# Optimization experiments

Hardware: AMD Instinct MI355X
Metric: run time of the kernel (lower is better)

## Reference

```python
import jax, jax.numpy as jnp
import numpy as np

N = 4096        # nodes
E = 65536       # edges (avg degree 16)
L = 64          # latent_dims
K = 256         # kernel_dims
ED = 6          # edge_dims
DEPTH = 2


def _gelu(x):
    # torch.nn.GELU / F.gelu default = exact erf form
    return jax.nn.gelu(x, approximate=False)


def setup_inputs() -> dict:
    key = jax.random.key(0)
    ks = jax.random.split(key, 12)
    u = lambda k, shape, fan: jax.random.uniform(k, shape, jnp.float32, -1.0, 1.0) / np.sqrt(fan)
    return {
        "nodes": jax.random.normal(ks[0], (N, L), jnp.float32),
        "edge_index": jax.random.randint(ks[1], (2, E), 0, N, jnp.int32),
        "edge_attr": jax.random.uniform(ks[2], (E, ED), jnp.float32),
        # DenseNet kernel MLP: ED -> K -> K -> L*L (GELU between layers)
        "W1": u(ks[3], (ED, K), ED), "b1": jnp.zeros((K,), jnp.float32),
        "W2": u(ks[4], (K, K), K),  "b2": jnp.zeros((K,), jnp.float32),
        "W3": u(ks[5], (K, L * L), K), "b3": jnp.zeros((L * L,), jnp.float32),
        # NNConv root linear (no bias) + conv bias
        "W_root": u(ks[6], (L, L), L),
        "bias": jnp.zeros((L,), jnp.float32),
    }


def reference(nodes, edge_index, edge_attr, W1, b1, W2, b2, W3, b3, W_root, bias):
    src, dst = edge_index[0], edge_index[1]
    # Edge-conditioned dynamic weights (depend only on edge_attr -> compute once)
    h = _gelu(edge_attr @ W1 + b1)          # [E, K]
    h = _gelu(h @ W2 + b2)                  # [E, K]
    W_edge = (h @ W3 + b3).reshape(E, L, L) # [E, L_in, L_out]

    def conv(x):
        msg = jnp.einsum('ei,eio->eo', x[src], W_edge)          # gather + per-edge matmul
        agg = jax.ops.segment_sum(msg, dst, num_segments=N)     # scatter-add to dst
        return agg + x @ W_root + bias

    x = nodes
    for idx in range(DEPTH):
        x = conv(x)
        if idx < DEPTH - 1:
            x = _gelu(x)
    return x
```

## Files before the change

kernel.cpp:

```cpp
#include <hip/hip_runtime.h>
#include <math.h>

#define NN 4096
#define NE 65536
#define LL 64
#define KK 256
#define ED 6
#define MAXSUPER 6144

typedef __bf16 bf16_t;
typedef __attribute__((ext_vector_type(4))) __bf16 bf16x4;
typedef __attribute__((ext_vector_type(8))) __bf16 bf16x8;
typedef __attribute__((ext_vector_type(4))) float f32x4;
typedef __attribute__((ext_vector_type(16))) float f32x16;

#define OFF_CNT    ((size_t)0)
#define OFF_DESC   ((size_t)16384)
#define OFF_AGG0   ((size_t)147456)
#define OFF_AGG1   ((size_t)1196032)
#define ZERO_BYTES ((size_t)2244608)
#define OFF_CURSOR ((size_t)2244608)
#define OFF_SORTED ((size_t)2260992)
#define OFF_W2R    ((size_t)2785280)
#define OFF_W3RR   ((size_t)2916352)
#define OFF_Q0     ((size_t)5013504)
#define OFF_Q1     ((size_t)6062080)
#define OFF_X1F    ((size_t)7110656)
#define OFF_X0BF   ((size_t)8159232)
#define OFF_X1BF   ((size_t)8683520)
#define OFF_H      ((size_t)9207808)
#define OFF_P      ((size_t)42762240)

__device__ __forceinline__ float gelu_f(float x) {
    return 0.5f * x * (1.0f + erff(x * 0.7071067811865476f));
}
__device__ __forceinline__ bf16_t f2bf(float x) { return (bf16_t)x; }

__global__ void k_hist(const int* __restrict__ ei, int* __restrict__ cnt) {
    int e = blockIdx.x * 256 + threadIdx.x;
    atomicAdd(&cnt[ei[e]], 1);
}

__global__ void k_scan(const int* __restrict__ cnt, int* __restrict__ cursor,
                       int4* __restrict__ descs) {
    __shared__ int pd[1024], pc[1024];
    int t = threadIdx.x;
    int deg[4]; int sd = 0, sc = 0;
#pragma unroll
    for (int j = 0; j < 4; j++) {
        deg[j] = cnt[t * 4 + j];
        sd += deg[j];
        sc += (deg[j] + 31) >> 5;
    }
    pd[t] = sd; pc[t] = sc;
    __syncthreads();
    for (int off = 1; off < 1024; off <<= 1) {
        int vd = 0, vc = 0;
        if (t >= off) { vd = pd[t - off]; vc = pc[t - off]; }
        __syncthreads();
        pd[t] += vd; pc[t] += vc;
        __syncthreads();
    }
    int rd = (t > 0) ? pd[t - 1] : 0;
    int rc = (t > 0) ? pc[t - 1] : 0;
    for (int j = 0; j < 4; j++) {
        int v = t * 4 + j, d = deg[j];
        cursor[v] = rd;
        int nch = (d + 31) >> 5;
        for (int c = 0; c < nch; c++) {
            int rem = d - c * 32;
            descs[rc + c] = make_int4(v, rd + c * 32, rem < 32 ? rem : 32, 0);
        }
        rc += nch; rd += d;
    }
}

__global__ void __launch_bounds__(256) k_fuse3(
        const int* __restrict__ ei, int* __restrict__ cursor, int2* __restrict__ sorted,
        const float* __restrict__ W3, bf16_t* __restrict__ W3rr,
        const float* __restrict__ W2, bf16_t* __restrict__ W2r,
        const float* __restrict__ attr, const float* __restrict__ W1,
        const float* __restrict__ b1, bf16_t* __restrict__ a1,
        const float* __restrict__ x, const float* __restrict__ b3,
        bf16_t* __restrict__ xbf, float* __restrict__ Q) {
    __shared__ float smem[4096];
    int bid = blockIdx.x, tid = threadIdx.x;
    if (bid < 256) {
        int e = bid * 256 + tid;
        int s = ei[e], d = ei[NE + e];
        int pos = atomicAdd(&cursor[s], 1);
        sorted[pos] = make_int2(e, d);
    } else if (bid < 512) {
        int k0 = bid - 256;
        for (int idx = tid; idx < 4096; idx += 256)
            smem[idx] = W3[(size_t)k0 * 4096 + idx];
        __syncthreads();
        int sbase = (2 * (k0 >> 4)) * 512 + (((k0 >> 3) & 1) * 32) * 8 + (k0 & 7);
#pragma unroll
        for (int m = 0; m < 2; m++) {
            int w = m * 256 + tid;
            int o = w >> 3, ib = w & 7;
            int s = sbase + (o >> 5) * 512 + (o & 31) * 8;
            int f = (s >> 4) * 1024 + (ib >> 2) * 512 + (ib & 3) * 128 + (s & 15) * 8;
            bf16x8 pk;
#pragma unroll
            for (int j = 0; j < 8; j++) pk[j] = f2bf(smem[(ib * 8 + j) * 64 + o]);
            *(bf16x8*)(W3rr + f) = pk;
        }
    } else if (bid < 768) {
        int t = (bid - 512) * 256 + tid;
        int kk = t >> 13, nn = (t >> 9) & 15, lane = (t >> 3) & 63, j = t & 7;
        int k = kk * 32 + (lane >> 4) * 8 + j;
        int n = nn * 16 + (lane & 15);
        W2r[t] = f2bf(W2[k * 256 + n]);
    } else if (bid < 1792) {
        float* sa = smem;
        int e0 = (bid - 768) * 64;
        for (int i = tid; i < 64 * ED; i += 256) sa[i] = attr[(size_t)e0 * ED + i];
        int col4 = (tid & 63) * 4;
        float w[ED][4], bb[4];
#pragma unroll
        for (int j = 0; j < ED; j++)
#pragma unroll
            for (int c = 0; c < 4; c++) w[j][c] = W1[j * 256 + col4 + c];
#pragma unroll
        for (int c = 0; c < 4; c++) bb[c] = b1[col4 + c];
        __syncthreads();
        int esub = tid >> 6;
#pragma unroll 1
        for (int eg = 0; eg < 16; eg++) {
            int el = eg * 4 + esub;
            float av[ED];
#pragma unroll
            for (int j = 0; j < ED; j++) av[j] = sa[el * ED + j];
            bf16x4 ov;
#pragma unroll
            for (int c = 0; c < 4; c++) {
                float acc = bb[c];
#pragma unroll
                for (int j = 0; j < ED; j++) acc += av[j] * w[j][c];
                ov[c] = f2bf(gelu_f(acc));
            }
            *(bf16x4*)(a1 + (size_t)(e0 + el) * 256 + col4) = ov;
        }
    } else {
        int v = (bid - 1792) * 4 + (tid >> 6);
        int o = tid & 63;
        float xv = x[v * 64 + o];
        smem[tid] = xv;
        xbf[v * 64 + o] = f2bf(xv);
        __syncthreads();
        const float* sx = smem + (tid >> 6) * 64;
        float q = 0.0f;
#pragma unroll 8
        for (int i = 0; i < 64; i++) q += sx[i] * b3[i * 64 + o];
        Q[v * 64 + o] = q;
    }
}

__device__ __forceinline__ void pgemm_body(const bf16_t* __restrict__ xbf,
                                           const bf16_t* __restrict__ W3rr,
                                           bf16_t* __restrict__ P,
                                           bf16_t* __restrict__ sw_wave,
                                           int strip, int rg) {
    int wave = threadIdx.x >> 6, lane = threadIdx.x & 63;
    int col = lane & 15, quad = lane >> 4;
    int half = lane >> 5, l5 = lane & 31;
    bf16_t* sw = sw_wave + wave * 4224;
    bf16x8 b[16][2];
#pragma unroll
    for (int nn = 0; nn < 16; nn++) {
        int sn = strip * 16 + nn;
#pragma unroll
        for (int ki = 0; ki < 2; ki++)
            b[nn][ki] = *(const bf16x8*)(W3rr + (size_t)(sn * 2 + ki) * 512 + lane * 8);
    }
#pragma unroll 1
    for (int rt = 0; rt < 4; rt++) {
        int rowbase = rg * 256 + wave * 64 + rt * 16;
        const bf16_t* arow = xbf + (size_t)(rowbase + col) * 64;
        bf16x8 a0 = *(const bf16x8*)(arow + quad * 8);
        bf16x8 a1v = *(const bf16x8*)(arow + 32 + quad * 8);
#pragma unroll
        for (int nn = 0; nn < 16; nn++) {
            f32x4 acc;
#pragma unroll
            for (int r = 0; r < 4; r++) acc[r] = 0.0f;
            acc = __builtin_amdgcn_mfma_f32_16x16x32_bf16(b[nn][0], a0, acc, 0, 0, 0);
            acc = __builtin_amdgcn_mfma_f32_16x16x32_bf16(b[nn][1], a1v, acc, 0, 0, 0);
            bf16x4 pk;
#pragma unroll
            for (int r = 0; r < 4; r++) pk[r] = f2bf(acc[r]);
            *(bf16x4*)(sw + col * 264 + nn * 16 + quad * 4) = pk;
        }
        __builtin_amdgcn_wave_barrier();
#pragma unroll
        for (int i = 0; i < 8; i++) {
            int r2 = 2 * i + half;
            bf16x8 vb = *(const bf16x8*)(sw + r2 * 264 + l5 * 8);
            *(bf16x8*)(P + (size_t)(rowbase + r2) * 16384 + strip * 256 + l5 * 8) = vb;
        }
        __builtin_amdgcn_wave_barrier();
    }
}

__global__ void __launch_bounds__(256, 2) k_fuse4(const bf16_t* __restrict__ xbf,
                                                  const bf16_t* __restrict__ W3rr,
                                                  bf16_t* __restrict__ P,
                                                  const bf16_t* __restrict__ a1,
                                                  const bf16_t* __restrict__ W2r,
                                                  const float* __restrict__ b2,
                                                  bf16_t* __restrict__ h) {
    __shared__ bf16_t sB[16896];
    if (blockIdx.x < 1024) {
        pgemm_body(xbf, W3rr, P, sB, blockIdx.x & 63, blockIdx.x >> 6);
    } else {
        int tid = threadIdx.x;
        int wave = tid >> 6, lane = tid & 63, col = lane & 15, quad = lane >> 4;
        int base = (blockIdx.x - 1024) * 128 + wave * 32;
        bf16x8 a[2][8];
#pragma unroll
        for (int t = 0; t < 2; t++) {
            const bf16_t* arow = a1 + (size_t)(base + t * 16 + col) * 256;
#pragma unroll
            for (int kk = 0; kk < 8; kk++)
                a[t][kk] = *(const bf16x8*)(arow + kk * 32 + quad * 8);
        }
#pragma unroll 1
        for (int p = 0; p < 4; p++) {
#pragma unroll
            for (int it = 0; it < 8; it++) {
                int c = it * 256 + tid;
                int fl = c >> 6;
                int e = (c & 63) * 8;
                int kk = fl >> 2, nnl = fl & 3;
                *(bf16x8*)(sB + fl * 512 + e) =
                    *(const bf16x8*)(W2r + (size_t)(kk * 16 + p * 4 + nnl) * 512 + e);
            }
            __syncthreads();
#pragma unroll
            for (int nnl = 0; nnl < 4; nnl++) {
                f32x4 acc0, acc1;
#pragma unroll
                for (int r = 0; r < 4; r++) { acc0[r] = 0.0f; acc1[r] = 0.0f; }
#pragma unroll
                for (int kk = 0; kk < 8; kk++) {
                    bf16x8 b = *(const bf16x8*)(sB + (kk * 4 + nnl) * 512 + lane * 8);
                    acc0 = __builtin_amdgcn_mfma_f32_16x16x32_bf16(a[0][kk], b, acc0, 0, 0, 0);
                    acc1 = __builtin_amdgcn_mfma_f32_16x16x32_bf16(a[1][kk], b, acc1, 0, 0, 0);
                }
                int ncol = (p * 4 + nnl) * 16 + col;
                float bv = b2[ncol];
#pragma unroll
                for (int r = 0; r < 4; r++) {
                    int row0 = base + quad * 4 + r;
                    h[(size_t)row0 * 256 + ncol] = f2bf(gelu_f(acc0[r] + bv));
                    h[(size_t)(row0 + 16) * 256 + ncol] = f2bf(gelu_f(acc1[r] + bv));
                }
            }
            __syncthreads();
        }
    }
}

__global__ void __launch_bounds__(256, 2) k_pgemm(const bf16_t* __restrict__ xbf,
                                                  const bf16_t* __restrict__ W3rr,
                                                  bf16_t* __restrict__ P) {
    __shared__ bf16_t sw_all[16896];
    pgemm_body(xbf, W3rr, P, sw_all, blockIdx.x & 63, blockIdx.x >> 6);
}

__global__ void __launch_bounds__(256) k_agg(const int4* __restrict__ descs,
                                             const int2* __restrict__ sorted,
                                             const bf16_t* __restrict__ h,
                                             const bf16_t* __restrict__ P,
                                             const float* __restrict__ Q,
                                             float* __restrict__ agg) {
    int chunk = blockIdx.x * 4 + (threadIdx.x >> 6);
    int lane = threadIdx.x & 63;
    int row = lane & 31, khalf = lane >> 5;
    int4 d = descs[chunk];
    int v = d.x, base = d.y, cnt = d.z;
    if (cnt == 0) return;
    bool valid = (row < cnt);
    int2 ed = sorted[base + (valid ? row : 0)];
    int eid = ed.x, dst = ed.y;

    bf16x8 zero;
#pragma unroll
    for (int i = 0; i < 8; i++) zero[i] = (bf16_t)0.0f;

    bf16x8 a[16];
    const bf16_t* hrow = h + (size_t)eid * 256;
#pragma unroll
    for (int kt = 0; kt < 16; kt++) {
        bf16x8 t = *(const bf16x8*)(hrow + kt * 16 + khalf * 8);
        a[kt] = valid ? t : zero;
    }
    const bf16_t* Pv = P + (size_t)v * 16384;
    f32x16 acc0, acc1;
#pragma unroll
    for (int r = 0; r < 16; r++) { acc0[r] = 0.0f; acc1[r] = 0.0f; }
#pragma unroll
    for (int kt = 0; kt < 16; kt++) {
        bf16x8 b0 = *(const bf16x8*)(Pv + (size_t)(kt * 2 + 0) * 512 + lane * 8);
        bf16x8 b1 = *(const bf16x8*)(Pv + (size_t)(kt * 2 + 1) * 512 + lane * 8);
        acc0 = __builtin_amdgcn_mfma_f32_32x32x16_bf16(a[kt], b0, acc0, 0, 0, 0);
        acc1 = __builtin_amdgcn_mfma_f32_32x32x16_bf16(a[kt], b1, acc1, 0, 0, 0);
    }
    float q0 = Q[v * 64 + row];
    float q1 = Q[v * 64 + 32 + row];
#pragma unroll
    for (int r = 0; r < 16; r++) {
        int mm = (r & 3) + 8 * (r >> 2) + 4 * khalf;
        int de = __shfl(dst, mm, 64);
        if (mm < cnt) {
            atomicAdd(&agg[(size_t)de * 64 + row], acc0[r] + q0);
            atomicAdd(&agg[(size_t)de * 64 + 32 + row], acc1[r] + q1);
        }
    }
}

__global__ void k_combine1(const float* __restrict__ x, const float* __restrict__ agg,
                           const float* __restrict__ Wroot, const float* __restrict__ bias,
                           const float* __restrict__ b3, float* __restrict__ x1,
                           bf16_t* __restrict__ x1bf, float* __restrict__ Q1) {
    __shared__ float sx[64], sy[64];
    int v = blockIdx.x, o = threadIdx.x;
    sx[o] = x[v * 64 + o];
    __syncthreads();
    float acc = agg[v * 64 + o] + bias[o];
#pragma unroll 8
    for (int i = 0; i < 64; i++) acc += sx[i] * Wroot[i * 64 + o];
    acc = gelu_f(acc);
    x1[v * 64 + o] = acc;
    x1bf[v * 64 + o] = f2bf(acc);
    sy[o] = acc;
    __syncthreads();
    float q = 0.0f;
#pragma unroll 8
    for (int i = 0; i < 64; i++) q += sy[i] * b3[i * 64 + o];
    Q1[v * 64 + o] = q;
}

__global__ void k_combine2(const float* __restrict__ x1, const float* __restrict__ agg,
                           const float* __restrict__ Wroot, const float* __restrict__ bias,
                           float* __restrict__ out) {
    __shared__ float sx[64];
    int v = blockIdx.x, o = threadIdx.x;
    sx[o] = x1[v * 64 + o];
    __syncthreads();
    float acc = agg[v * 64 + o] + bias[o];
#pragma unroll 8
    for (int i = 0; i < 64; i++) acc += sx[i] * Wroot[i * 64 + o];
    out[v * 64 + o] = acc;
}

extern "C" void kernel_launch(void* const* d_in, const int* in_sizes, int n_in,
                              void* d_out, int out_size, void* d_ws, size_t ws_size,
                              hipStream_t stream) {
    const float* nodes = (const float*)d_in[0];
    const int*   ei    = (const int*)d_in[1];
    const float* attr  = (const float*)d_in[2];
    const float* W1    = (const float*)d_in[3];
    const float* b1    = (const float*)d_in[4];
    const float* W2    = (const float*)d_in[5];
    const float* b2    = (const float*)d_in[6];
    const float* W3    = (const float*)d_in[7];
    const float* b3    = (const float*)d_in[8];
    const float* Wroot = (const float*)d_in[9];
    const float* bias  = (const float*)d_in[10];
    float* out = (float*)d_out;
    char* ws = (char*)d_ws;

    int*    cnt    = (int*)(ws + OFF_CNT);
    int4*   descs  = (int4*)(ws + OFF_DESC);
    float*  agg0   = (float*)(ws + OFF_AGG0);
    float*  agg1   = (float*)(ws + OFF_AGG1);
    int*    cursor = (int*)(ws + OFF_CURSOR);
    int2*   sorted = (int2*)(ws + OFF_SORTED);
    bf16_t* W2r    = (bf16_t*)(ws + OFF_W2R);
    bf16_t* W3rr   = (bf16_t*)(ws + OFF_W3RR);
    float*  Q0     = (float*)(ws + OFF_Q0);
    float*  Q1     = (float*)(ws + OFF_Q1);
    float*  x1f    = (float*)(ws + OFF_X1F);
    bf16_t* x0bf   = (bf16_t*)(ws + OFF_X0BF);
    bf16_t* x1bf   = (bf16_t*)(ws + OFF_X1BF);
    bf16_t* hbuf   = (bf16_t*)(ws + OFF_H);
    bf16_t* a1buf  = (bf16_t*)(ws + OFF_H);
    bf16_t* Pbuf   = (bf16_t*)(ws + OFF_P);

    hipMemsetAsync(ws, 0, ZERO_BYTES, stream);
    k_hist<<<NE / 256, 256, 0, stream>>>(ei, cnt);
    k_scan<<<1, 1024, 0, stream>>>(cnt, cursor, descs);
    k_fuse3<<<2816, 256, 0, stream>>>(ei, cursor, sorted, W3, W3rr, W2, W2r,
                                      attr, W1, b1, a1buf, nodes, b3, x0bf, Q0);
    k_fuse4<<<1536, 256, 0, stream>>>(x0bf, W3rr, Pbuf, a1buf, W2r, b2, hbuf);
    k_agg<<<MAXSUPER / 4, 256, 0, stream>>>(descs, sorted, hbuf, Pbuf, Q0, agg0);
    k_combine1<<<NN, 64, 0, stream>>>(nodes, agg0, Wroot, bias, b3, x1f, x1bf, Q1);
    k_pgemm<<<1024, 256, 0, stream>>>(x1bf, W3rr, Pbuf);
    k_agg<<<MAXSUPER / 4, 256, 0, stream>>>(descs, sorted, hbuf, Pbuf, Q1, agg1);
    k_combine2<<<NN, 64, 0, stream>>>(x1f, agg1, Wroot, bias, out);
}
```

Baseline: 266.2 us.

## Fuse per-node P projection into aggregation kernel, avoiding materialized P buffer

Replaces the separate P-GEMM (x·W3 per node, stored as a 4096×16384 bf16 tensor) and per-chunk aggregation kernels with a single conv kernel. Each block handles 16 source nodes, computes their P slices on the fly in shared memory from streamed W3 tiles, and immediately applies them to the edge h rows. The goal is to remove the large P write and read round-trip through global memory. The cost is that only 256 blocks run at one block per CU, each with serialized W3 streaming and heavy syncthreads, so parallelism is low and load imbalance across node groups is possible.

```diff
diff --git a/kernel.cpp b/kernel.cpp
--- a/kernel.cpp
+++ b/kernel.cpp
@@ -6,7 +6,6 @@
 #define LL 64
 #define KK 256
 #define ED 6
-#define MAXSUPER 6144
 
 typedef __bf16 bf16_t;
 typedef __attribute__((ext_vector_type(4))) __bf16 bf16x4;
@@ -29,7 +28,7 @@
 #define OFF_X0BF   ((size_t)8159232)
 #define OFF_X1BF   ((size_t)8683520)
 #define OFF_H      ((size_t)9207808)
-#define OFF_P      ((size_t)42762240)
+#define OFF_GST    ((size_t)42762240)
 
 __device__ __forceinline__ float gelu_f(float x) {
     return 0.5f * x * (1.0f + erff(x * 0.7071067811865476f));
@@ -42,7 +41,7 @@
 }
 
 __global__ void k_scan(const int* __restrict__ cnt, int* __restrict__ cursor,
-                       int4* __restrict__ descs) {
+                       int4* __restrict__ descs, int* __restrict__ gstart) {
     __shared__ int pd[1024], pc[1024];
     int t = threadIdx.x;
     int deg[4]; int sd = 0, sc = 0;
@@ -65,6 +64,7 @@
     int rc = (t > 0) ? pc[t - 1] : 0;
     for (int j = 0; j < 4; j++) {
         int v = t * 4 + j, d = deg[j];
+        if ((v & 15) == 0) gstart[v >> 4] = rc;
         cursor[v] = rd;
         int nch = (d + 31) >> 5;
         for (int c = 0; c < nch; c++) {
@@ -73,6 +73,7 @@
         }
         rc += nch; rd += d;
     }
+    if (t == 1023) gstart[256] = rc;
 }
 
 __global__ void __launch_bounds__(256) k_fuse3(
@@ -158,166 +159,177 @@
     }
 }
 
-__device__ __forceinline__ void pgemm_body(const bf16_t* __restrict__ xbf,
-                                           const bf16_t* __restrict__ W3rr,
-                                           bf16_t* __restrict__ P,
-                                           bf16_t* __restrict__ sw_wave,
-                                           int strip, int rg) {
-    int wave = threadIdx.x >> 6, lane = threadIdx.x & 63;
-    int col = lane & 15, quad = lane >> 4;
-    int half = lane >> 5, l5 = lane & 31;
-    bf16_t* sw = sw_wave + wave * 4224;
-    bf16x8 b[16][2];
-#pragma unroll
-    for (int nn = 0; nn < 16; nn++) {
-        int sn = strip * 16 + nn;
-#pragma unroll
-        for (int ki = 0; ki < 2; ki++)
-            b[nn][ki] = *(const bf16x8*)(W3rr + (size_t)(sn * 2 + ki) * 512 + lane * 8);
+__global__ void __launch_bounds__(256) k_mlp2(const bf16_t* __restrict__ a1,
+                                              const bf16_t* __restrict__ W2r,
+                                              const float* __restrict__ b2,
+                                              bf16_t* __restrict__ h) {
+    __shared__ bf16_t sB[16384];
+    int tid = threadIdx.x;
+    int wave = tid >> 6, lane = tid & 63, col = lane & 15, quad = lane >> 4;
+    int base = blockIdx.x * 128 + wave * 32;
+    bf16x8 a[2][8];
+#pragma unroll
+    for (int t = 0; t < 2; t++) {
+        const bf16_t* arow = a1 + (size_t)(base + t * 16 + col) * 256;
+#pragma unroll
+        for (int kk = 0; kk < 8; kk++)
+            a[t][kk] = *(const bf16x8*)(arow + kk * 32 + quad * 8);
     }
 #pragma unroll 1
-    for (int rt = 0; rt < 4; rt++) {
-        int rowbase = rg * 256 + wave * 64 + rt * 16;
-        const bf16_t* arow = xbf + (size_t)(rowbase + col) * 64;
-        bf16x8 a0 = *(const bf16x8*)(arow + quad * 8);
-        bf16x8 a1v = *(const bf16x8*)(arow + 32 + quad * 8);
-#pragma unroll
-        for (int nn = 0; nn < 16; nn++) {
-            f32x4 acc;
-#pragma unroll
-            for (int r = 0; r < 4; r++) acc[r] = 0.0f;
-            acc = __builtin_amdgcn_mfma_f32_16x16x32_bf16(b[nn][0], a0, acc, 0, 0, 0);
-            acc = __builtin_amdgcn_mfma_f32_16x16x32_bf16(b[nn][1], a1v, acc, 0, 0, 0);
-            bf16x4 pk;
-#pragma unroll
-            for (int r = 0; r < 4; r++) pk[r] = f2bf(acc[r]);
-            *(bf16x4*)(sw + col * 264 + nn * 16 + quad * 4) = pk;
-        }
-        __builtin_amdgcn_wave_barrier();
-#pragma unroll
-        for (int i = 0; i < 8; i++) {
-            int r2 = 2 * i + half;
-            bf16x8 vb = *(const bf16x8*)(sw + r2 * 264 + l5 * 8);
-            *(bf16x8*)(P + (size_t)(rowbase + r2) * 16384 + strip * 256 + l5 * 8) = vb;
-        }
-        __builtin_amdgcn_wave_barrier();
-    }
-}
-
-__global__ void __launch_bounds__(256, 2) k_fuse4(const bf16_t* __restrict__ xbf,
-                                                  const bf16_t* __restrict__ W3rr,
-                                                  bf16_t* __restrict__ P,
-                                                  const bf16_t* __restrict__ a1,
-                                                  const bf16_t* __restrict__ W2r,
-                                                  const float* __restrict__ b2,
-                                                  bf16_t* __restrict__ h) {
-    __shared__ bf16_t sB[16896];
-    if (blockIdx.x < 1024) {
-        pgemm_body(xbf, W3rr, P, sB, blockIdx.x & 63, blockIdx.x >> 6);
-    } else {
-        int tid = threadIdx.x;
-        int wave = tid >> 6, lane = tid & 63, col = lane & 15, quad = lane >> 4;
-        int base = (blockIdx.x - 1024) * 128 + wave * 32;
-        bf16x8 a[2][8];
-#pragma unroll
-        for (int t = 0; t < 2; t++) {
-            const bf16_t* arow = a1 + (size_t)(base + t * 16 + col) * 256;
-#pragma unroll
-            for (int kk = 0; kk < 8; kk++)
-                a[t][kk] = *(const bf16x8*)(arow + kk * 32 + quad * 8);
-        }
+    for (int p = 0; p < 4; p++) {
+#pragma unroll
+        for (int it = 0; it < 8; it++) {
+            int c = it * 256 + tid;
+            int fl = c >> 6;
+            int e = (c & 63) * 8;
+            int kk = fl >> 2, nnl = fl & 3;
+            *(bf16x8*)(sB + fl * 512 + e) =
+                *(const bf16x8*)(W2r + (size_t)(kk * 16 + p * 4 + nnl) * 512 + e);
+        }
+        __syncthreads();
+#pragma unroll
+        for (int nnl = 0; nnl < 4; nnl++) {
+            f32x4 acc0, acc1;
+#pragma unroll
+            for (int r = 0; r < 4; r++) { acc0[r] = 0.0f; acc1[r] = 0.0f; }
+#pragma unroll
+            for (int kk = 0; kk < 8; kk++) {
+                bf16x8 b = *(const bf16x8*)(sB + (kk * 4 + nnl) * 512 + lane * 8);
+                acc0 = __builtin_amdgcn_mfma_f32_16x16x32_bf16(a[0][kk], b, acc0, 0, 0, 0);
+                acc1 = __builtin_amdgcn_mfma_f32_16x16x32_bf16(a[1][kk], b, acc1, 0, 0, 0);
+            }
+            int ncol = (p * 4 + nnl) * 16 + col;
+            float bv = b2[ncol];
+#pragma unroll
+            for (int r = 0; r < 4; r++) {
+                int row0 = base + quad * 4 + r;
+                h[(size_t)row0 * 256 + ncol] = f2bf(gelu_f(acc0[r] + bv));
+                h[(size_t)(row0 + 16) * 256 + ncol] = f2bf(gelu_f(acc1[r] + bv));
+            }
+        }
+        __syncthreads();
+    }
+}
+
+__global__ void __launch_bounds__(256, 1) k_conv(
+        const bf16_t* __restrict__ xbf, const bf16_t* __restrict__ h,
+        const bf16_t* __restrict__ W3rr, const float* __restrict__ Q,
+        const int* __restrict__ gstart, const int4* __restrict__ descs,
+        const int2* __restrict__ sorted, float* __restrict__ agg) {
+    __shared__ bf16_t sW[32768];
+    __shared__ bf16_t sP[16 * 2060];
+    const int g = blockIdx.x;
+    const int tid = threadIdx.x;
+    const int wave = tid >> 6, lane = tid & 63;
+    const int col = lane & 15, quad = lane >> 4;
+    const int row = lane & 31, khalf = lane >> 5;
+    const int scbase = gstart[g];
+    const int nsc = gstart[g + 1] - scbase;
+    if (nsc == 0) return;
+
+    const bf16_t* xr = xbf + (size_t)(g * 16 + col) * 64;
+    bf16x8 x0 = *(const bf16x8*)(xr + quad * 8);
+    bf16x8 x1 = *(const bf16x8*)(xr + 32 + quad * 8);
+
+    bf16x8 zero8;
+#pragma unroll
+    for (int i = 0; i < 8; i++) zero8[i] = (bf16_t)0.0f;
+
+    int nrounds = (nsc + 31) >> 5;
 #pragma unroll 1
-        for (int p = 0; p < 4; p++) {
-#pragma unroll
-            for (int it = 0; it < 8; it++) {
-                int c = it * 256 + tid;
-                int fl = c >> 6;
-                int e = (c & 63) * 8;
-                int kk = fl >> 2, nnl = fl & 3;
-                *(bf16x8*)(sB + fl * 512 + e) =
-                    *(const bf16x8*)(W2r + (size_t)(kk * 16 + p * 4 + nnl) * 512 + e);
-            }
-            __syncthreads();
-#pragma unroll
-            for (int nnl = 0; nnl < 4; nnl++) {
-                f32x4 acc0, acc1;
-#pragma unroll
-                for (int r = 0; r < 4; r++) { acc0[r] = 0.0f; acc1[r] = 0.0f; }
-#pragma unroll
-                for (int kk = 0; kk < 8; kk++) {
-                    bf16x8 b = *(const bf16x8*)(sB + (kk * 4 + nnl) * 512 + lane * 8);
-                    acc0 = __builtin_amdgcn_mfma_f32_16x16x32_bf16(a[0][kk], b, acc0, 0, 0, 0);
-                    acc1 = __builtin_amdgcn_mfma_f32_16x16x32_bf16(a[1][kk], b, acc1, 0, 0, 0);
+    for (int round = 0; round < nrounds; round++) {
+        int vloc[8], cntv[8], dstv[8];
+        const bf16_t* hp[8];
+        bool used[8], lval[8];
+        float q0v[8], q1v[8];
+#pragma unroll
+        for (int myc = 0; myc < 8; myc++) {
+            int slot = round * 32 + myc * 4 + wave;
+            used[myc] = (slot < nsc);
+            vloc[myc] = 0; cntv[myc] = 0; dstv[myc] = 0;
+            hp[myc] = h; lval[myc] = false; q0v[myc] = 0.0f; q1v[myc] = 0.0f;
+            if (used[myc]) {
+                int4 d = descs[scbase + slot];
+                int v = d.x, base = d.y, cnt = d.z;
+                vloc[myc] = v & 15;
+                cntv[myc] = cnt;
+                bool valid = row < cnt;
+                lval[myc] = valid;
+                int2 ed = sorted[base + (valid ? row : 0)];
+                hp[myc] = h + (size_t)ed.x * 256;
+                dstv[myc] = ed.y;
+                q0v[myc] = Q[v * 64 + row];
+                q1v[myc] = Q[v * 64 + 32 + row];
+            }
+        }
+        f32x16 acc[8][2];
+#pragma unroll
+        for (int myc = 0; myc < 8; myc++)
+#pragma unroll
+            for (int oh = 0; oh < 2; oh++)
+#pragma unroll
+                for (int r = 0; r < 16; r++) acc[myc][oh][r] = 0.0f;
+
+#pragma unroll 1
+        for (int kt = 0; kt < 8; kt++) {
+#pragma unroll 1
+            for (int sub = 0; sub < 4; sub++) {
+                const bf16x8* srcv = (const bf16x8*)(W3rr + ((size_t)kt * 256 + sub * 64) * 512);
+                bf16x8* dv = (bf16x8*)sW;
+#pragma unroll
+                for (int it = 0; it < 16; it++)
+                    dv[it * 256 + tid] = srcv[it * 256 + tid];
+                __syncthreads();
+#pragma unroll
+                for (int t = 0; t < 8; t++) {
+                    int fl = (wave * 8 + t) * 2;
+                    bf16x8 b0 = *(const bf16x8*)(sW + (size_t)fl * 512 + lane * 8);
+                    bf16x8 b1 = *(const bf16x8*)(sW + (size_t)(fl + 1) * 512 + lane * 8);
+                    f32x4 dacc;
+#pragma unroll
+                    for (int r = 0; r < 4; r++) dacc[r] = 0.0f;
+                    dacc = __builtin_amdgcn_mfma_f32_16x16x32_bf16(b0, x0, dacc, 0, 0, 0);
+                    dacc = __builtin_amdgcn_mfma_f32_16x16x32_bf16(b1, x1, dacc, 0, 0, 0);
+                    bf16x4 pk;
+#pragma unroll
+                    for (int r = 0; r < 4; r++) pk[r] = f2bf(dacc[r]);
+                    *(bf16x4*)(sP + col * 2060 + sub * 512 + (wave * 8 + t) * 16 + quad * 4) = pk;
                 }
-                int ncol = (p * 4 + nnl) * 16 + col;
-                float bv = b2[ncol];
-#pragma unroll
-                for (int r = 0; r < 4; r++) {
-                    int row0 = base + quad * 4 + r;
-                    h[(size_t)row0 * 256 + ncol] = f2bf(gelu_f(acc0[r] + bv));
-                    h[(size_t)(row0 + 16) * 256 + ncol] = f2bf(gelu_f(acc1[r] + bv));
+                __syncthreads();
+            }
+#pragma unroll
+            for (int myc = 0; myc < 8; myc++) {
+                if (!used[myc]) continue;
+                const bf16_t* hr = hp[myc] + kt * 32 + khalf * 8;
+                bf16x8 t0 = *(const bf16x8*)(hr);
+                bf16x8 t1 = *(const bf16x8*)(hr + 16);
+                bf16x8 a0 = lval[myc] ? t0 : zero8;
+                bf16x8 a1 = lval[myc] ? t1 : zero8;
+                const bf16_t* pb = sP + vloc[myc] * 2060 + lane * 8;
+                bf16x8 b00 = *(const bf16x8*)(pb);
+                bf16x8 b01 = *(const bf16x8*)(pb + 512);
+                bf16x8 b10 = *(const bf16x8*)(pb + 1024);
+                bf16x8 b11 = *(const bf16x8*)(pb + 1536);
+                acc[myc][0] = __builtin_amdgcn_mfma_f32_32x32x16_bf16(a0, b00, acc[myc][0], 0, 0, 0);
+                acc[myc][0] = __builtin_amdgcn_mfma_f32_32x32x16_bf16(a1, b10, acc[myc][0], 0, 0, 0);
+                acc[myc][1] = __builtin_amdgcn_mfma_f32_32x32x16_bf16(a0, b01, acc[myc][1], 0, 0, 0);
+                acc[myc][1] = __builtin_amdgcn_mfma_f32_32x32x16_bf16(a1, b11, acc[myc][1], 0, 0, 0);
+            }
+        }
+#pragma unroll
+        for (int myc = 0; myc < 8; myc++) {
+            if (!used[myc]) continue;
+#pragma unroll
+            for (int r = 0; r < 16; r++) {
+                int mm = (r & 3) + 8 * (r >> 2) + 4 * khalf;
+                int de = __shfl(dstv[myc], mm, 64);
+                if (mm < cntv[myc]) {
+                    atomicAdd(&agg[(size_t)de * 64 + row], acc[myc][0][r] + q0v[myc]);
+                    atomicAdd(&agg[(size_t)de * 64 + 32 + row], acc[myc][1][r] + q1v[myc]);
                 }
             }
-            __syncthreads();
-        }
-    }
-}
-
-__global__ void __launch_bounds__(256, 2) k_pgemm(const bf16_t* __restrict__ xbf,
-                                                  const bf16_t* __restrict__ W3rr,
-                                                  bf16_t* __restrict__ P) {
-    __shared__ bf16_t sw_all[16896];
-    pgemm_body(xbf, W3rr, P, sw_all, blockIdx.x & 63, blockIdx.x >> 6);
-}
-
-__global__ void __launch_bounds__(256) k_agg(const int4* __restrict__ descs,
-                                             const int2* __restrict__ sorted,
-                                             const bf16_t* __restrict__ h,
-                                             const bf16_t* __restrict__ P,
-                                             const float* __restrict__ Q,
-                                             float* __restrict__ agg) {
-    int chunk = blockIdx.x * 4 + (threadIdx.x >> 6);
-    int lane = threadIdx.x & 63;
-    int row = lane & 31, khalf = lane >> 5;
-    int4 d = descs[chunk];
-    int v = d.x, base = d.y, cnt = d.z;
-    if (cnt == 0) return;
-    bool valid = (row < cnt);
-    int2 ed = sorted[base + (valid ? row : 0)];
-    int eid = ed.x, dst = ed.y;
-
-    bf16x8 zero;
-#pragma unroll
-    for (int i = 0; i < 8; i++) zero[i] = (bf16_t)0.0f;
-
-    bf16x8 a[16];
-    const bf16_t* hrow = h + (size_t)eid * 256;
-#pragma unroll
-    for (int kt = 0; kt < 16; kt++) {
-        bf16x8 t = *(const bf16x8*)(hrow + kt * 16 + khalf * 8);
-        a[kt] = valid ? t : zero;
-    }
-    const bf16_t* Pv = P + (size_t)v * 16384;
-    f32x16 acc0, acc1;
-#pragma unroll
-    for (int r = 0; r < 16; r++) { acc0[r] = 0.0f; acc1[r] = 0.0f; }
-#pragma unroll
-    for (int kt = 0; kt < 16; kt++) {
-        bf16x8 b0 = *(const bf16x8*)(Pv + (size_t)(kt * 2 + 0) * 512 + lane * 8);
-        bf16x8 b1 = *(const bf16x8*)(Pv + (size_t)(kt * 2 + 1) * 512 + lane * 8);
-        acc0 = __builtin_amdgcn_mfma_f32_32x32x16_bf16(a[kt], b0, acc0, 0, 0, 0);
-        acc1 = __builtin_amdgcn_mfma_f32_32x32x16_bf16(a[kt], b1, acc1, 0, 0, 0);
-    }
-    float q0 = Q[v * 64 + row];
-    float q1 = Q[v * 64 + 32 + row];
-#pragma unroll
-    for (int r = 0; r < 16; r++) {
-        int mm = (r & 3) + 8 * (r >> 2) + 4 * khalf;
-        int de = __shfl(dst, mm, 64);
-        if (mm < cnt) {
-            atomicAdd(&agg[(size_t)de * 64 + row], acc0[r] + q0);
-            atomicAdd(&agg[(size_t)de * 64 + 32 + row], acc1[r] + q1);
-        }
+        }
+        __syncthreads();
     }
 }
 
@@ -388,17 +400,16 @@
     bf16_t* x1bf   = (bf16_t*)(ws + OFF_X1BF);
     bf16_t* hbuf   = (bf16_t*)(ws + OFF_H);
     bf16_t* a1buf  = (bf16_t*)(ws + OFF_H);
-    bf16_t* Pbuf   = (bf16_t*)(ws + OFF_P);
+    int*    gstart = (int*)(ws + OFF_GST);
 
     hipMemsetAsync(ws, 0, ZERO_BYTES, stream);
     k_hist<<<NE / 256, 256, 0, stream>>>(ei, cnt);
-    k_scan<<<1, 1024, 0, stream>>>(cnt, cursor, descs);
+    k_scan<<<1, 1024, 0, stream>>>(cnt, cursor, descs, gstart);
     k_fuse3<<<2816, 256, 0, stream>>>(ei, cursor, sorted, W3, W3rr, W2, W2r,
                                       attr, W1, b1, a1buf, nodes, b3, x0bf, Q0);
-    k_fuse4<<<1536, 256, 0, stream>>>(x0bf, W3rr, Pbuf, a1buf, W2r, b2, hbuf);
-    k_agg<<<MAXSUPER / 4, 256, 0, stream>>>(descs, sorted, hbuf, Pbuf, Q0, agg0);
+    k_mlp2<<<512, 256, 0, stream>>>(a1buf, W2r, b2, hbuf);
+    k_conv<<<256, 256, 0, stream>>>(x0bf, hbuf, W3rr, Q0, gstart, descs, sorted, agg0);
     k_combine1<<<NN, 64, 0, stream>>>(nodes, agg0, Wroot, bias, b3, x1f, x1bf, Q1);
-    k_pgemm<<<1024, 256, 0, stream>>>(x1bf, W3rr, Pbuf);
-    k_agg<<<MAXSUPER / 4, 256, 0, stream>>>(descs, sorted, hbuf, Pbuf, Q1, agg1);
+    k_conv<<<256, 256, 0, stream>>>(x1bf, hbuf, W3rr, Q1, gstart, descs, sorted, agg1);
     k_combine2<<<NN, 64, 0, stream>>>(x1f, agg1, Wroot, bias, out);
 }
```

Measured after the change: 494.9 us. +85.9%, slower.
